# Performance work log

Measured on AMD Instinct MI355X. Metric: run time of the kernel, lower is better.

Reference implementation:

```python
import jax, jax.numpy as jnp
import numpy as np

B = 8            # requests
TOK = 4096       # new tokens per request (prefill)
PAGE = 16        # page_size
PAGES_PER = TOK // PAGE   # 256 pages per request
NPAGES = 4096    # max_num_pages
H, D = 8, 128    # kv heads, head_dim


def setup_inputs() -> dict:
    key = jax.random.key(0)
    kk, kv_, kp = jax.random.split(key, 3)
    T = B * TOK
    k = jax.random.normal(kk, (T, H, D), dtype=jnp.float32)
    v = jax.random.normal(kv_, (T, H, D), dtype=jnp.float32)
    kv_cache = jnp.zeros((NPAGES, 2, PAGE, H, D), dtype=jnp.float32)
    # each request appends TOK tokens into PAGES_PER fresh pages, last page full
    kv_append_indptr = (jnp.arange(B + 1) * TOK).astype(jnp.int32)
    kv_page_indptr = (jnp.arange(B + 1) * PAGES_PER).astype(jnp.int32)
    kv_page_indices = jax.random.permutation(kp, NPAGES)[: B * PAGES_PER].astype(jnp.int32)
    kv_page_lastlen = jnp.full((B,), PAGE, dtype=jnp.int32)
    return {
        "k": k, "v": v, "kv_cache": kv_cache,
        "kv_append_indptr": kv_append_indptr,
        "kv_page_indices": kv_page_indices,
        "kv_page_indptr": kv_page_indptr,
        "kv_page_lastlen": kv_page_lastlen,
        "page_size": PAGE,
    }


def reference(k, v, kv_cache, kv_append_indptr, kv_page_indices,
              kv_page_indptr, kv_page_lastlen, page_size):
    # Paged KV-cache append (flashinfer append_paged_kv_cache semantics):
    # new tokens of request i occupy the LAST (indptr[i+1]-indptr[i]) logical
    # positions of its page list, where the sequence length after append is
    # (num_pages_i - 1) * page_size + lastlen_i.
    T = k.shape[0]
    t = jnp.arange(T)
    # per-token request id via ragged indptr
    b = jnp.searchsorted(kv_append_indptr, t, side="right") - 1  # [T]
    num_new = kv_append_indptr[b + 1] - kv_append_indptr[b]
    num_pages = kv_page_indptr[b + 1] - kv_page_indptr[b]
    seq_len = (num_pages - 1) * page_size + kv_page_lastlen[b]
    # logical position of each new token within its request's sequence
    pos = seq_len - num_new + (t - kv_append_indptr[b])          # [T]
    page = kv_page_indices[kv_page_indptr[b] + pos // page_size]  # [T] physical page
    slot = pos % page_size                                        # [T] slot in page
    cache = kv_cache.at[page, 0, slot].set(k)
    cache = cache.at[page, 1, slot].set(v)
    return cache
```

## Files before the change

### kernel.cpp

```cpp
#include <hip/hip_runtime.h>

#define PAGE_SZ 16
#define ROW_FLOATS 1024
#define ROW_F4 256
#define ROWS_PER_PAGE 32
#define ELEMS_PER_PAGE 32768

__global__ void init_map_kernel(int2* __restrict__ map, int npages) {
    int i = blockIdx.x * blockDim.x + threadIdx.x;
    if (i < npages) map[i] = make_int2(-1, 0);
}

__global__ void fill_map_kernel(const int* __restrict__ append_indptr,
                                const int* __restrict__ page_indices,
                                const int* __restrict__ page_indptr,
                                const int* __restrict__ lastlen,
                                int2* __restrict__ map,
                                int B, int max_entries) {
    int idx = blockIdx.x * blockDim.x + threadIdx.x;
    if (idx >= max_entries) return;
    if (idx >= page_indptr[B]) return;
    int b = 0;
    while (page_indptr[b + 1] <= idx) b++;
    int j         = idx - page_indptr[b];
    int num_pages = page_indptr[b + 1] - page_indptr[b];
    int num_new   = append_indptr[b + 1] - append_indptr[b];
    int seq_len   = (num_pages - 1) * PAGE_SZ + lastlen[b];
    int start     = seq_len - num_new;
    int pos0      = j * PAGE_SZ;
    int lo = pos0 > start ? pos0 : start;
    int hi = (pos0 + PAGE_SZ) < seq_len ? (pos0 + PAGE_SZ) : seq_len;
    if (lo >= hi) return;
    int p = page_indices[idx];
    if (pos0 >= start && pos0 + PAGE_SZ <= seq_len) {
        map[p] = make_int2(1, append_indptr[b] + pos0 - start);
    } else {
        map[p] = make_int2(2, (b << 20) | j);
    }
}

__global__ void gather_kernel(const float4* __restrict__ k,
                              const float4* __restrict__ v,
                              const float4* __restrict__ cache_in,
                              const int* __restrict__ append_indptr,
                              const int* __restrict__ page_indptr,
                              const int* __restrict__ lastlen,
                              const int2* __restrict__ map,
                              float4* __restrict__ out) {
    int bid   = blockIdx.x;
    int page  = bid >> 5;
    int row   = bid & 31;
    int kvsel = row >> 4;
    int slot  = row & 15;
    int tid   = threadIdx.x;
    long e4   = (long)bid * ROW_F4 + tid;

    int2 m = map[page];
    float4 val;
    if (m.x == 1) {
        long t = (long)(m.y + slot);
        const float4* src = kvsel ? v : k;
        val = src[t * ROW_F4 + tid];
    } else if (m.x < 0) {
        val = cache_in[e4];
    } else {
        int b = m.y >> 20, j = m.y & 0xFFFFF;
        int num_pages = page_indptr[b + 1] - page_indptr[b];
        int num_new   = append_indptr[b + 1] - append_indptr[b];
        int seq_len   = (num_pages - 1) * PAGE_SZ + lastlen[b];
        int start     = seq_len - num_new;
        int pos       = j * PAGE_SZ + slot;
        if (pos >= start && pos < seq_len) {
            long t = (long)(append_indptr[b] + pos - start);
            const float4* src = kvsel ? v : k;
            val = src[t * ROW_F4 + tid];
        } else {
            val = cache_in[e4];
        }
    }
    out[e4] = val;
}

extern "C" void kernel_launch(void* const* d_in, const int* in_sizes, int n_in,
                              void* d_out, int out_size, void* d_ws, size_t ws_size,
                              hipStream_t stream) {
    const float4* k        = (const float4*)d_in[0];
    const float4* v        = (const float4*)d_in[1];
    const float4* cache_in = (const float4*)d_in[2];
    const int* append_indptr = (const int*)d_in[3];
    const int* page_indices  = (const int*)d_in[4];
    const int* page_indptr   = (const int*)d_in[5];
    const int* lastlen       = (const int*)d_in[6];

    int B           = in_sizes[3] - 1;
    int max_entries = in_sizes[4];
    int npages      = (int)((long)out_size / ELEMS_PER_PAGE);

    int2* map = (int2*)d_ws;

    init_map_kernel<<<(npages + 255) / 256, 256, 0, stream>>>(map, npages);
    fill_map_kernel<<<(max_entries + 255) / 256, 256, 0, stream>>>(
        append_indptr, page_indices, page_indptr, lastlen, map, B, max_entries);
    gather_kernel<<<npages * ROWS_PER_PAGE, 256, 0, stream>>>(
        k, v, cache_in, append_indptr, page_indptr, lastlen, map,
        (float4*)d_out);
}
```

Before: 194.2 us.

## Replace per-row gather grid with grid-stride kernel unrolled four loads deep

The one-block-per-row gather launch (131072 blocks) becomes a fixed 2048-block grid-stride kernel. Each thread issues four independent 16-byte loads before its stores, to raise memory-level parallelism and cut block scheduling overhead. Per-element map lookups and index math are recomputed from the flat index, which adds some integer work and loses the per-block uniform page decode.

```diff
diff --git a/kernel.cpp b/kernel.cpp
--- a/kernel.cpp
+++ b/kernel.cpp
@@ -1,10 +1,11 @@
 #include <hip/hip_runtime.h>
 
 #define PAGE_SZ 16
-#define ROW_FLOATS 1024
 #define ROW_F4 256
-#define ROWS_PER_PAGE 32
+#define PAGE_F4 8192
 #define ELEMS_PER_PAGE 32768
+
+typedef float f32x4 __attribute__((ext_vector_type(4)));
 
 __global__ void init_map_kernel(int2* __restrict__ map, int npages) {
     int i = blockIdx.x * blockDim.x + threadIdx.x;
@@ -39,69 +40,77 @@
     }
 }
 
-__global__ void gather_kernel(const float4* __restrict__ k,
-                              const float4* __restrict__ v,
-                              const float4* __restrict__ cache_in,
-                              const int* __restrict__ append_indptr,
-                              const int* __restrict__ page_indptr,
-                              const int* __restrict__ lastlen,
-                              const int2* __restrict__ map,
-                              float4* __restrict__ out) {
-    int bid   = blockIdx.x;
-    int page  = bid >> 5;
-    int row   = bid & 31;
-    int kvsel = row >> 4;
-    int slot  = row & 15;
-    int tid   = threadIdx.x;
-    long e4   = (long)bid * ROW_F4 + tid;
+struct GatherArgs {
+    const f32x4* k;
+    const f32x4* v;
+    const f32x4* cache_in;
+    const int* append_indptr;
+    const int* page_indptr;
+    const int* lastlen;
+    const int2* map;
+};
 
-    int2 m = map[page];
-    float4 val;
+__device__ __forceinline__ f32x4 load_src(long e4, const GatherArgs& a) {
+    int page = (int)(e4 >> 13);
+    int2 m = a.map[page];
+    if (m.x < 0) return a.cache_in[e4];
+    int row  = (int)((e4 >> 8) & 31);
+    int slot = row & 15;
+    const f32x4* src = (row >> 4) ? a.v : a.k;
     if (m.x == 1) {
-        long t = (long)(m.y + slot);
-        const float4* src = kvsel ? v : k;
-        val = src[t * ROW_F4 + tid];
-    } else if (m.x < 0) {
-        val = cache_in[e4];
-    } else {
-        int b = m.y >> 20, j = m.y & 0xFFFFF;
-        int num_pages = page_indptr[b + 1] - page_indptr[b];
-        int num_new   = append_indptr[b + 1] - append_indptr[b];
-        int seq_len   = (num_pages - 1) * PAGE_SZ + lastlen[b];
-        int start     = seq_len - num_new;
-        int pos       = j * PAGE_SZ + slot;
-        if (pos >= start && pos < seq_len) {
-            long t = (long)(append_indptr[b] + pos - start);
-            const float4* src = kvsel ? v : k;
-            val = src[t * ROW_F4 + tid];
-        } else {
-            val = cache_in[e4];
-        }
+        return src[((long)(m.y + slot) << 8) | (e4 & 255)];
     }
-    out[e4] = val;
+    int b = m.y >> 20, j = m.y & 0xFFFFF;
+    int num_pages = a.page_indptr[b + 1] - a.page_indptr[b];
+    int num_new   = a.append_indptr[b + 1] - a.append_indptr[b];
+    int seq_len   = (num_pages - 1) * PAGE_SZ + a.lastlen[b];
+    int start     = seq_len - num_new;
+    int pos       = j * PAGE_SZ + slot;
+    if (pos >= start && pos < seq_len) {
+        return src[((long)(a.append_indptr[b] + pos - start) << 8) | (e4 & 255)];
+    }
+    return a.cache_in[e4];
+}
+
+__global__ void __launch_bounds__(256)
+gather_stride_kernel(GatherArgs a, f32x4* __restrict__ out, long total) {
+    const long stride = (long)gridDim.x * blockDim.x;
+    long e = (long)blockIdx.x * blockDim.x + threadIdx.x;
+    for (; e + 3 * stride < total; e += 4 * stride) {
+        f32x4 v0 = load_src(e,              a);
+        f32x4 v1 = load_src(e +     stride, a);
+        f32x4 v2 = load_src(e + 2 * stride, a);
+        f32x4 v3 = load_src(e + 3 * stride, a);
+        out[e]              = v0;
+        out[e +     stride] = v1;
+        out[e + 2 * stride] = v2;
+        out[e + 3 * stride] = v3;
+    }
+    for (; e < total; e += stride) out[e] = load_src(e, a);
 }
 
 extern "C" void kernel_launch(void* const* d_in, const int* in_sizes, int n_in,
                               void* d_out, int out_size, void* d_ws, size_t ws_size,
                               hipStream_t stream) {
-    const float4* k        = (const float4*)d_in[0];
-    const float4* v        = (const float4*)d_in[1];
-    const float4* cache_in = (const float4*)d_in[2];
-    const int* append_indptr = (const int*)d_in[3];
-    const int* page_indices  = (const int*)d_in[4];
-    const int* page_indptr   = (const int*)d_in[5];
-    const int* lastlen       = (const int*)d_in[6];
+    GatherArgs a;
+    a.k        = (const f32x4*)d_in[0];
+    a.v        = (const f32x4*)d_in[1];
+    a.cache_in = (const f32x4*)d_in[2];
+    a.append_indptr = (const int*)d_in[3];
+    const int* page_indices = (const int*)d_in[4];
+    a.page_indptr   = (const int*)d_in[5];
+    a.lastlen       = (const int*)d_in[6];
 
     int B           = in_sizes[3] - 1;
     int max_entries = in_sizes[4];
     int npages      = (int)((long)out_size / ELEMS_PER_PAGE);
+    long total_f4   = (long)out_size / 4;
 
     int2* map = (int2*)d_ws;
+    a.map = map;
 
     init_map_kernel<<<(npages + 255) / 256, 256, 0, stream>>>(map, npages);
     fill_map_kernel<<<(max_entries + 255) / 256, 256, 0, stream>>>(
-        append_indptr, page_indices, page_indptr, lastlen, map, B, max_entries);
-    gather_kernel<<<npages * ROWS_PER_PAGE, 256, 0, stream>>>(
-        k, v, cache_in, append_indptr, page_indptr, lastlen, map,
-        (float4*)d_out);
+        a.append_indptr, page_indices, a.page_indptr, a.lastlen, map, B, max_entries);
+    gather_stride_kernel<<<2048, 256, 0, stream>>>(a, (f32x4*)d_out, total_f4);
 }
```

Result: slower. 224.5 us (+15.6%).
